# Optimization experiments

Measured on AMD Instinct MI355X. Metric: run time of the kernel, lower is better.

The kernel has to match this reference:

```python
import jax, jax.numpy as jnp
import numpy as np

N_NODES = 50000
N_EDGES = 800000
DIM = 128  # in_dim == out_dim (required by the original module's math)
BN_EPS = 1e-5


def setup_inputs() -> dict:
    key = jax.random.key(0)
    ks = jax.random.split(key, 12)
    d = DIM
    s = 1.0 / np.sqrt(d)
    x = jax.random.normal(ks[0], (N_NODES, d), dtype=jnp.float32)
    edge_index = jax.random.randint(ks[1], (2, N_EDGES), 0, N_NODES, dtype=jnp.int64)
    # message_fn: Linear(in_dim, out_dim)
    W_msg = jax.random.uniform(ks[2], (d, d), jnp.float32, -s, s)
    b_msg = jax.random.uniform(ks[3], (d,), jnp.float32, -s, s)
    # attention: Linear(2*in_dim, 1)
    sa = 1.0 / np.sqrt(2 * d)
    W_att = jax.random.uniform(ks[4], (2 * d, 1), jnp.float32, -sa, sa)
    b_att = jax.random.uniform(ks[5], (1,), jnp.float32, -sa, sa)
    # GRUCell(out_dim, out_dim): weight_ih [3d, d], weight_hh [3d, d]
    W_ih = jax.random.uniform(ks[6], (3 * d, d), jnp.float32, -s, s)
    b_ih = jax.random.uniform(ks[7], (3 * d,), jnp.float32, -s, s)
    W_hh = jax.random.uniform(ks[8], (3 * d, d), jnp.float32, -s, s)
    b_hh = jax.random.uniform(ks[9], (3 * d,), jnp.float32, -s, s)
    # BatchNorm1d(out_dim)
    gamma = jnp.ones((d,), jnp.float32)
    beta = jnp.zeros((d,), jnp.float32)
    return {"x": x, "edge_index": edge_index, "W_msg": W_msg, "b_msg": b_msg,
            "W_att": W_att, "b_att": b_att, "W_ih": W_ih, "b_ih": b_ih,
            "W_hh": W_hh, "b_hh": b_hh, "gamma": gamma, "beta": beta}


def reference(x, edge_index, W_msg, b_msg, W_att, b_att, W_ih, b_ih, W_hh, b_hh, gamma, beta):
    num_nodes, d = x.shape
    src = edge_index[0]
    dst = edge_index[1]
    xs = x[src]            # [E, d] gather
    xd = x[dst]            # [E, d] gather
    # sigmoid(cat([xs, xd]) @ W_att + b_att) without materializing the concat
    att = jax.nn.sigmoid(xs @ W_att[:d] + xd @ W_att[d:] + b_att)  # [E, 1]
    messages = (xs @ W_msg + b_msg) * att                          # [E, d]
    aggregated = jax.ops.segment_sum(messages, dst, num_segments=num_nodes)  # scatter-add
    # GRUCell(aggregated, x)
    gi = aggregated @ W_ih.T + b_ih   # [N, 3d]
    gh = x @ W_hh.T + b_hh            # [N, 3d]
    i_r, i_z, i_n = jnp.split(gi, 3, axis=1)
    h_r, h_z, h_n = jnp.split(gh, 3, axis=1)
    r = jax.nn.sigmoid(i_r + h_r)
    z = jax.nn.sigmoid(i_z + h_z)
    n = jnp.tanh(i_n + r * h_n)
    h_new = (1.0 - z) * n + z * x
    # dropout is identity in eval mode; BatchNorm1d in training mode (batch stats, biased var)
    mean = jnp.mean(h_new, axis=0)
    var = jnp.var(h_new, axis=0)
    return gamma * (h_new - mean) * jax.lax.rsqrt(var + BN_EPS) + beta
```

## Files before the change

kernel.cpp:

```cpp
#include <hip/hip_runtime.h>
#include <hip/hip_bf16.h>

#define DIM 128
#define SWS 136
typedef __hip_bfloat16 bf16;
typedef __attribute__((ext_vector_type(8))) short bf16x8;
typedef __attribute__((ext_vector_type(4))) float f32x4;

__device__ __forceinline__ float b2f(bf16 v) { return __bfloat162float(v); }
__device__ __forceinline__ bf16  f2b(float v) { return __float2bfloat16(v); }

template<bool F32>
__device__ __forceinline__ float ldf(const void* p, size_t i) {
    if (F32) return ((const float*)p)[i];
    else     return b2f(((const bf16*)p)[i]);
}
template<bool F32>
__device__ __forceinline__ void stf(void* p, size_t i, float v) {
    if (F32) ((float*)p)[i] = v;
    else     ((bf16*)p)[i] = f2b(v);
}

__device__ __forceinline__ bf16x8 pack8_f32(const float* p) {
    bf16x8 r;
#pragma unroll
    for (int i = 0; i < 8; ++i) { bf16 t = f2b(p[i]); r[i] = *(const short*)&t; }
    return r;
}
template<bool F32>
__device__ __forceinline__ bf16x8 load_frag(const void* base, size_t off) {
    if (F32) return pack8_f32((const float*)base + off);
    else     return *(const bf16x8*)((const unsigned short*)base + off);
}

__device__ __forceinline__ float bflo(unsigned int m) { return __uint_as_float(m << 16); }
__device__ __forceinline__ float bfhi(unsigned int m) { return __uint_as_float(m & 0xFFFF0000u); }

__device__ __forceinline__ float sigmoidf_fast(float v) { return 1.0f / (1.0f + __expf(-v)); }
__device__ __forceinline__ float tanhf_fast(float t) {
    float e2 = __expf(2.0f * t);
    return 1.0f - 2.0f / (e2 + 1.0f);
}

__global__ void detect_kernel(const void* __restrict__ ei, const void* __restrict__ gamma,
                              int n_nodes, int* __restrict__ flags)
{
    if (blockIdx.x == 0 && threadIdx.x == 0) {
        const long long* e64 = (const long long*)ei;
        int ok = 1;
        for (int i = 0; i < 16; ++i) {
            long long v = e64[i];
            if (v < 0 || v >= (long long)n_nodes) ok = 0;
        }
        flags[0] = ok;
        const float* g = (const float*)gamma;
        flags[1] = (fabsf(g[0] - 1.0f) < 1e-6f && fabsf(g[1] - 1.0f) < 1e-6f) ? 1 : 0;
    }
}

__device__ void atomic_add_bf16(bf16* addr, float val)
{
    unsigned int* base = (unsigned int*)((size_t)addr & ~(size_t)3);
    bool hi = ((size_t)addr & 2) != 0;
    unsigned int old = *base, assumed;
    do {
        assumed = old;
        unsigned short cur = hi ? (unsigned short)(assumed >> 16) : (unsigned short)(assumed & 0xFFFF);
        bf16 cb = *(bf16*)&cur;
        bf16 nb = f2b(b2f(cb) + val);
        unsigned short ns = *(unsigned short*)&nb;
        unsigned int newv = hi ? ((assumed & 0x0000FFFFu) | ((unsigned int)ns << 16))
                               : ((assumed & 0xFFFF0000u) | (unsigned int)ns);
        old = atomicCAS(base, assumed, newv);
    } while (old != assumed);
}

#define NW (144 * 128)
#define NI (384 * 128)
__global__ __launch_bounds__(256) void prep_weights_kernel(
    const void* __restrict__ W_msg, const void* __restrict__ W_att,
    const void* __restrict__ W_ih, const void* __restrict__ W_hh,
    unsigned short* __restrict__ wbuf, const int* __restrict__ flags)
{
    bool f32 = flags[1] != 0;
    int i = blockIdx.x * blockDim.x + threadIdx.x;
    if (i >= NW + 2 * NI) return;
    float v;
    if (i < NW) {
        int j = i >> 7, k = i & 127;
        if (j < 128)       v = f32 ? ((const float*)W_msg)[k * 128 + j] : b2f(((const bf16*)W_msg)[k * 128 + j]);
        else if (j == 128) v = f32 ? ((const float*)W_att)[k]           : b2f(((const bf16*)W_att)[k]);
        else if (j == 129) v = f32 ? ((const float*)W_att)[128 + k]     : b2f(((const bf16*)W_att)[128 + k]);
        else               v = 0.0f;
    } else if (i < NW + NI) {
        int t = i - NW;
        v = f32 ? ((const float*)W_ih)[t] : b2f(((const bf16*)W_ih)[t]);
    } else {
        int t = i - NW - NI;
        v = f32 ? ((const float*)W_hh)[t] : b2f(((const bf16*)W_hh)[t]);
    }
    bf16 b = f2b(v);
    wbuf[i] = *(unsigned short*)&b;
}

template<bool F32>
__device__ void node_mfma_body(unsigned short* __restrict__ sw,
                               const void* __restrict__ x, const unsigned short* __restrict__ Wnode,
                               const void* __restrict__ b_msg, unsigned short* __restrict__ Mb,
                               float* __restrict__ a_src, float* __restrict__ a_dst, int n_nodes)
{
    int wave = threadIdx.x >> 6, lane = threadIdx.x & 63;
    int m0 = (blockIdx.x * 8 + wave) * 16;
    int mrow = lane & 15, quad = lane >> 4;
    bool active = (m0 < n_nodes);
    int mnode = active ? (m0 + mrow < n_nodes ? m0 + mrow : n_nodes - 1) : 0;

    {
        int t = threadIdx.x;
#pragma unroll
        for (int i = 0; i < 5; ++i) {
            int v = t + i * 512;
            if (v < 2304) {
                int row = v >> 4, col = (v & 15) * 8;
                *(bf16x8*)(sw + row * SWS + col) = *(const bf16x8*)(Wnode + row * DIM + col);
            }
        }
    }

    bf16x8 a[4];
#pragma unroll
    for (int kq = 0; kq < 4; ++kq)
        a[kq] = load_frag<F32>(x, (size_t)mnode * DIM + kq * 32 + quad * 8);

    __syncthreads();

#pragma unroll
    for (int jt = 0; jt < 9; ++jt) {
        const unsigned short* wr = sw + (jt * 16 + mrow) * SWS + quad * 8;
        bf16x8 B[4];
#pragma unroll
        for (int kq = 0; kq < 4; ++kq)
            B[kq] = *(const bf16x8*)(wr + kq * 32);
        f32x4 acc = {0, 0, 0, 0};
#pragma unroll
        for (int kq = 0; kq < 4; ++kq)
            acc = __builtin_amdgcn_mfma_f32_16x16x32_bf16(a[kq], B[kq], acc, 0, 0, 0);
        if (!active) continue;
        if (jt < 8) {
            int jcol = jt * 16 + mrow;
            float bm = ldf<F32>(b_msg, jcol);
#pragma unroll
            for (int rg = 0; rg < 4; ++rg) {
                int node = m0 + quad * 4 + rg;
                if (node < n_nodes) {
                    bf16 bb = f2b(acc[rg] + bm);
                    Mb[(size_t)node * DIM + jcol] = *(unsigned short*)&bb;
                }
            }
        } else if (mrow < 2) {
#pragma unroll
            for (int rg = 0; rg < 4; ++rg) {
                int node = m0 + quad * 4 + rg;
                if (node < n_nodes) {
                    if (mrow == 0) a_src[node] = acc[rg];
                    else           a_dst[node] = acc[rg];
                }
            }
        }
    }
}

__global__ __launch_bounds__(512) void node_mfma_kernel(
    const void* x, const unsigned short* Wnode, const void* b_msg,
    unsigned short* Mb, float* a_src, float* a_dst, int n_nodes, const int* __restrict__ flags)
{
    __shared__ unsigned short sw[144 * SWS];
    if (flags[1]) node_mfma_body<true>(sw, x, Wnode, b_msg, Mb, a_src, a_dst, n_nodes);
    else          node_mfma_body<false>(sw, x, Wnode, b_msg, Mb, a_src, a_dst, n_nodes);
}

__global__ __launch_bounds__(256) void hist_kernel(
    const void* __restrict__ ei, int* __restrict__ deg, int n_edges, const int* __restrict__ flags)
{
    int i = blockIdx.x * blockDim.x + threadIdx.x;
    if (i >= n_edges) return;
    int t = flags[0] ? (int)((const long long*)ei)[n_edges + i] : ((const int*)ei)[n_edges + i];
    atomicAdd(&deg[t], 1);
}

__global__ __launch_bounds__(256) void partial_sum_kernel(
    const int* __restrict__ deg, int* __restrict__ partials, int n_nodes)
{
    __shared__ int s[256];
    int t = threadIdx.x;
    int i = blockIdx.x * 256 + t;
    s[t] = (i < n_nodes) ? deg[i] : 0;
    __syncthreads();
    for (int off = 128; off > 0; off >>= 1) {
        if (t < off) s[t] += s[t + off];
        __syncthreads();
    }
    if (t == 0) partials[blockIdx.x] = s[0];
}

__global__ __launch_bounds__(256) void partial_scan_kernel(
    int* __restrict__ partials, int nblocks)
{
    __shared__ int s[256];
    int t = threadIdx.x;
    int v = (t < nblocks) ? partials[t] : 0;
    s[t] = v;
    __syncthreads();
    for (int off = 1; off < 256; off <<= 1) {
        int u = (t >= off) ? s[t - off] : 0;
        __syncthreads();
        s[t] += u;
        __syncthreads();
    }
    if (t < nblocks) partials[t] = s[t] - v;
}

__global__ __launch_bounds__(256) void scan_write_kernel(
    const int* __restrict__ deg, const int* __restrict__ partials,
    int* __restrict__ row_start, int* __restrict__ fill, int n_nodes, int n_edges)
{
    __shared__ int s[256];
    int t = threadIdx.x;
    int i = blockIdx.x * 256 + t;
    int v = (i < n_nodes) ? deg[i] : 0;
    s[t] = v;
    __syncthreads();
    for (int off = 1; off < 256; off <<= 1) {
        int u = (t >= off) ? s[t - off] : 0;
        __syncthreads();
        s[t] += u;
        __syncthreads();
    }
    int excl = s[t] - v + partials[blockIdx.x];
    if (i < n_nodes) { row_start[i] = excl; fill[i] = excl; }
    if (blockIdx.x == 0 && t == 0) row_start[n_nodes] = n_edges;
}

__global__ __launch_bounds__(256) void scatter_kernel(
    const void* __restrict__ ei, const float* __restrict__ a_src, const float* __restrict__ a_dst,
    const void* __restrict__ b_att, int* __restrict__ fill,
    int* __restrict__ sorted_src, float* __restrict__ att,
    const int* __restrict__ flags, int n_edges)
{
    int i = blockIdx.x * blockDim.x + threadIdx.x;
    if (i >= n_edges) return;
    int s, t;
    if (flags[0]) {
        const long long* p = (const long long*)ei;
        s = (int)p[i]; t = (int)p[n_edges + i];
    } else {
        const int* p = (const int*)ei;
        s = p[i]; t = p[n_edges + i];
    }
    float battv = flags[1] ? ((const float*)b_att)[0] : b2f(((const bf16*)b_att)[0]);
    int pos = atomicAdd(&fill[t], 1);
    sorted_src[pos] = s;
    float logit = a_src[s] + a_dst[t] + battv;
    att[pos] = 1.0f / (1.0f + __expf(-logit));
}

__global__ __launch_bounds__(256) void aggregate_kernel(
    const unsigned short* __restrict__ Mb, const int* __restrict__ row_start,
    const int* __restrict__ sorted_src, const float* __restrict__ att,
    unsigned short* __restrict__ aggb, int n_nodes)
{
    int w = (int)((blockIdx.x * (unsigned)blockDim.x + threadIdx.x) >> 6);
    int lane = threadIdx.x & 63;
    if (w >= n_nodes) return;
    int beg = row_start[w], end = row_start[w + 1];
    float acc0 = 0.0f, acc1 = 0.0f;
    int e = beg;
    for (; e + 4 <= end; e += 4) {
        int s0 = sorted_src[e], s1 = sorted_src[e + 1], s2 = sorted_src[e + 2], s3 = sorted_src[e + 3];
        float w0 = att[e], w1 = att[e + 1], w2 = att[e + 2], w3 = att[e + 3];
        unsigned int m0 = *(const unsigned int*)(Mb + ((size_t)s0 << 7) + lane * 2);
        unsigned int m1 = *(const unsigned int*)(Mb + ((size_t)s1 << 7) + lane * 2);
        unsigned int m2 = *(const unsigned int*)(Mb + ((size_t)s2 << 7) + lane * 2);
        unsigned int m3 = *(const unsigned int*)(Mb + ((size_t)s3 << 7) + lane * 2);
        acc0 += w0 * bflo(m0) + w1 * bflo(m1) + w2 * bflo(m2) + w3 * bflo(m3);
        acc1 += w0 * bfhi(m0) + w1 * bfhi(m1) + w2 * bfhi(m2) + w3 * bfhi(m3);
    }
    for (; e < end; ++e) {
        int s = sorted_src[e];
        float a = att[e];
        unsigned int m = *(const unsigned int*)(Mb + ((size_t)s << 7) + lane * 2);
        acc0 += a * bflo(m);
        acc1 += a * bfhi(m);
    }
    bf16 r0 = f2b(acc0), r1 = f2b(acc1);
    unsigned int packed = (unsigned int)(*(unsigned short*)&r0) |
                          ((unsigned int)(*(unsigned short*)&r1) << 16);
    *(unsigned int*)(aggb + ((size_t)w << 7) + lane * 2) = packed;
}

template<bool F32>
__device__ void gru_mfma_body(unsigned short* __restrict__ sw,
                              const void* __restrict__ x, const unsigned short* __restrict__ aggb,
                              const unsigned short* __restrict__ Wih, const unsigned short* __restrict__ Whh,
                              const void* __restrict__ b_ih, const void* __restrict__ b_hh,
                              void* __restrict__ h_out, int n_nodes)
{
    int wave = threadIdx.x >> 6, lane = threadIdx.x & 63;
    int m0 = (blockIdx.x * 8 + wave) * 16;
    int mrow = lane & 15, quad = lane >> 4;
    bool active = (m0 < n_nodes);
    int mnode = active ? (m0 + mrow < n_nodes ? m0 + mrow : n_nodes - 1) : 0;

    bf16x8 a_ag[4], a_x[4];
#pragma unroll
    for (int kq = 0; kq < 4; ++kq) {
        a_ag[kq] = *(const bf16x8*)(aggb + (size_t)mnode * DIM + kq * 32 + quad * 8);
        a_x[kq]  = load_frag<F32>(x, (size_t)mnode * DIM + kq * 32 + quad * 8);
    }

    for (int jt = 0; jt < 8; ++jt) {
        {
            int t = threadIdx.x;
#pragma unroll
            for (int i = 0; i < 3; ++i) {
                int v = t + i * 512;
                int row = v >> 4;
                int col = (v & 15) * 8;
                int g   = row >> 4;
                int grow = row & 15;
                const unsigned short* srcm = (g < 3) ? Wih : Whh;
                const unsigned short* src = srcm + ((size_t)((g % 3) * 128 + jt * 16 + grow) * DIM + col);
                *(bf16x8*)(sw + row * SWS + col) = *(const bf16x8*)src;
            }
        }
        __syncthreads();

        f32x4 acc_ir = {0,0,0,0}, acc_iz = {0,0,0,0}, acc_in = {0,0,0,0};
        f32x4 acc_hr = {0,0,0,0}, acc_hz = {0,0,0,0}, acc_hn = {0,0,0,0};

#pragma unroll
        for (int half = 0; half < 2; ++half) {
            bf16x8 B[12];
#pragma unroll
            for (int kq = 0; kq < 2; ++kq) {
                int k = half * 2 + kq;
                int boff = mrow * SWS + k * 32 + quad * 8;
#pragma unroll
                for (int g = 0; g < 6; ++g)
                    B[kq * 6 + g] = *(const bf16x8*)(sw + g * (16 * SWS) + boff);
            }
#pragma unroll
            for (int kq = 0; kq < 2; ++kq) {
                int k = half * 2 + kq;
                acc_ir = __builtin_amdgcn_mfma_f32_16x16x32_bf16(a_ag[k], B[kq * 6 + 0], acc_ir, 0, 0, 0);
                acc_iz = __builtin_amdgcn_mfma_f32_16x16x32_bf16(a_ag[k], B[kq * 6 + 1], acc_iz, 0, 0, 0);
                acc_in = __builtin_amdgcn_mfma_f32_16x16x32_bf16(a_ag[k], B[kq * 6 + 2], acc_in, 0, 0, 0);
                acc_hr = __builtin_amdgcn_mfma_f32_16x16x32_bf16(a_x[k],  B[kq * 6 + 3], acc_hr, 0, 0, 0);
                acc_hz = __builtin_amdgcn_mfma_f32_16x16x32_bf16(a_x[k],  B[kq * 6 + 4], acc_hz, 0, 0, 0);
                acc_hn = __builtin_amdgcn_mfma_f32_16x16x32_bf16(a_x[k],  B[kq * 6 + 5], acc_hn, 0, 0, 0);
            }
        }
        __syncthreads();

        if (!active) continue;
        int jcol = jt * 16 + mrow;
        float xsv[4];
#pragma unroll
        for (int rg = 0; rg < 4; ++rg) {
            int node = m0 + quad * 4 + rg;
            int nclamp = node < n_nodes ? node : (n_nodes - 1);
            xsv[rg] = ldf<F32>(x, (size_t)nclamp * DIM + jcol);
        }
        float bir = ldf<F32>(b_ih, jcol), biz = ldf<F32>(b_ih, 128 + jcol), bin_ = ldf<F32>(b_ih, 256 + jcol);
        float bhr = ldf<F32>(b_hh, jcol), bhz = ldf<F32>(b_hh, 128 + jcol), bhn  = ldf<F32>(b_hh, 256 + jcol);
#pragma unroll
        for (int rg = 0; rg < 4; ++rg) {
            int node = m0 + quad * 4 + rg;
            if (node >= n_nodes) continue;
            float gir = acc_ir[rg] + bir, giz = acc_iz[rg] + biz, gin = acc_in[rg] + bin_;
            float ghr = acc_hr[rg] + bhr, ghz = acc_hz[rg] + bhz, ghn = acc_hn[rg] + bhn;
            float r = sigmoidf_fast(gir + ghr);
            float z = sigmoidf_fast(giz + ghz);
            float nn = tanhf_fast(gin + r * ghn);
            stf<F32>(h_out, (size_t)node * DIM + jcol, (1.0f - z) * nn + z * xsv[rg]);
        }
    }
}

__global__ __launch_bounds__(512) void gru_mfma_kernel(
    const void* x, const unsigned short* aggb, const unsigned short* Wih, const unsigned short* Whh,
    const void* b_ih, const void* b_hh, void* h_out, int n_nodes, const int* __restrict__ flags)
{
    __shared__ unsigned short sw[96 * SWS];
    if (flags[1]) gru_mfma_body<true>(sw, x, aggb, Wih, Whh, b_ih, b_hh, h_out, n_nodes);
    else          gru_mfma_body<false>(sw, x, aggb, Wih, Whh, b_ih, b_hh, h_out, n_nodes);
}

template<bool F32>
__device__ void node_pre_body(const void* __restrict__ x, const void* __restrict__ W_msg,
                              const void* __restrict__ b_msg, const void* __restrict__ W_att,
                              void* __restrict__ M, float* __restrict__ a_src,
                              float* __restrict__ a_dst)
{
    int n = blockIdx.x;
    int j = threadIdx.x;
    __shared__ float xs[DIM], r1[DIM], r2[DIM];
    float xv = ldf<F32>(x, (size_t)n * DIM + j);
    xs[j] = xv;
    r1[j] = xv * ldf<F32>(W_att, j);
    r2[j] = xv * ldf<F32>(W_att, DIM + j);
    __syncthreads();
    float acc = ldf<F32>(b_msg, j);
#pragma unroll 8
    for (int k = 0; k < DIM; ++k)
        acc += xs[k] * ldf<F32>(W_msg, (size_t)k * DIM + j);
    stf<F32>(M, (size_t)n * DIM + j, acc);
    for (int s = 64; s > 0; s >>= 1) {
        __syncthreads();
        if (j < s) { r1[j] += r1[j + s]; r2[j] += r2[j + s]; }
    }
    if (j == 0) { a_src[n] = r1[0]; a_dst[n] = r2[0]; }
}

__global__ __launch_bounds__(128) void node_pre_kernel(
    const void* x, const void* W_msg, const void* b_msg, const void* W_att,
    void* M, float* a_src, float* a_dst, const int* __restrict__ flags)
{
    if (flags[1]) node_pre_body<true>(x, W_msg, b_msg, W_att, M, a_src, a_dst);
    else          node_pre_body<false>(x, W_msg, b_msg, W_att, M, a_src, a_dst);
}

template<bool F32, bool AGGF32>
__device__ void edge_body(const void* __restrict__ ei, const void* __restrict__ M,
                          const float* __restrict__ a_src, const float* __restrict__ a_dst,
                          const void* __restrict__ b_att, void* __restrict__ agg,
                          int idx64, int n_edges)
{
    int e = (int)((blockIdx.x * (unsigned)blockDim.x + threadIdx.x) >> 6);
    int lane = threadIdx.x & 63;
    if (e >= n_edges) return;
    int s, t;
    if (idx64) {
        const long long* p = (const long long*)ei;
        s = (int)p[e]; t = (int)p[n_edges + e];
    } else {
        const int* p = (const int*)ei;
        s = p[e]; t = p[n_edges + e];
    }
    float logit = a_src[s] + a_dst[t] + ldf<F32>(b_att, 0);
    float attv = 1.0f / (1.0f + __expf(-logit));
    float m0 = ldf<F32>(M, (size_t)s * DIM + lane) * attv;
    float m1 = ldf<F32>(M, (size_t)s * DIM + 64 + lane) * attv;
    if (AGGF32) {
        float* a = (float*)agg;
        atomicAdd(&a[(size_t)t * DIM + lane], m0);
        atomicAdd(&a[(size_t)t * DIM + 64 + lane], m1);
    } else {
        bf16* a = (bf16*)agg;
        atomic_add_bf16(&a[(size_t)t * DIM + lane], m0);
        atomic_add_bf16(&a[(size_t)t * DIM + 64 + lane], m1);
    }
}

template<bool AGGF32>
__global__ __launch_bounds__(256) void edge_kernel(
    const void* ei, const void* M, const float* a_src, const float* a_dst,
    const void* b_att, void* agg, const int* __restrict__ flags, int n_edges)
{
    if (flags[1]) edge_body<true, AGGF32>(ei, M, a_src, a_dst, b_att, agg, flags[0], n_edges);
    else          edge_body<false, AGGF32>(ei, M, a_src, a_dst, b_att, agg, flags[0], n_edges);
}

#define NPB 8
template<bool F32, bool AGGF32>
__device__ void gru_body(const void* __restrict__ x, const void* __restrict__ agg,
                         const void* __restrict__ W_ih, const void* __restrict__ b_ih,
                         const void* __restrict__ W_hh, const void* __restrict__ b_hh,
                         void* __restrict__ h_new, int n_nodes)
{
    int node0 = blockIdx.x * NPB;
    int j = threadIdx.x;
    __shared__ float ag[NPB][DIM];
    __shared__ float xv[NPB][DIM];
    __shared__ float gi[NPB][3 * DIM];
    __shared__ float gh[NPB][3 * DIM];
    for (int i = j; i < NPB * DIM; i += 384) {
        int nn = i >> 7, d = i & 127;
        int node = node0 + nn;
        if (node < n_nodes) {
            ag[nn][d] = AGGF32 ? ((const float*)agg)[(size_t)node * DIM + d]
                               : b2f(((const bf16*)agg)[(size_t)node * DIM + d]);
            xv[nn][d] = ldf<F32>(x, (size_t)node * DIM + d);
        } else { ag[nn][d] = 0.0f; xv[nn][d] = 0.0f; }
    }
    __syncthreads();
    {
        float acc_i[NPB], acc_h[NPB];
        float bi = ldf<F32>(b_ih, j);
        float bh = ldf<F32>(b_hh, j);
#pragma unroll
        for (int m = 0; m < NPB; ++m) { acc_i[m] = bi; acc_h[m] = bh; }
#pragma unroll 4
        for (int k = 0; k < DIM; ++k) {
            float wik = ldf<F32>(W_ih, (size_t)j * DIM + k);
            float whk = ldf<F32>(W_hh, (size_t)j * DIM + k);
#pragma unroll
            for (int m = 0; m < NPB; ++m) {
                acc_i[m] += ag[m][k] * wik;
                acc_h[m] += xv[m][k] * whk;
            }
        }
#pragma unroll
        for (int m = 0; m < NPB; ++m) { gi[m][j] = acc_i[m]; gh[m][j] = acc_h[m]; }
    }
    __syncthreads();
    for (int i = j; i < NPB * DIM; i += 384) {
        int nn = i >> 7, d = i & 127;
        int node = node0 + nn;
        if (node >= n_nodes) continue;
        float r = 1.0f / (1.0f + __expf(-(gi[nn][d] + gh[nn][d])));
        float z = 1.0f / (1.0f + __expf(-(gi[nn][DIM + d] + gh[nn][DIM + d])));
        float nv = tanhf(gi[nn][2 * DIM + d] + r * gh[nn][2 * DIM + d]);
        float h = (1.0f - z) * nv + z * xv[nn][d];
        stf<F32>(h_new, (size_t)node * DIM + d, h);
    }
}

template<bool AGGF32>
__global__ __launch_bounds__(384) void gru_kernel(
    const void* x, const void* agg, const void* W_ih, const void* b_ih,
    const void* W_hh, const void* b_hh, void* h_new, int n_nodes,
    const int* __restrict__ flags)
{
    if (flags[1]) gru_body<true, AGGF32>(x, agg, W_ih, b_ih, W_hh, b_hh, h_new, n_nodes);
    else          gru_body<false, AGGF32>(x, agg, W_ih, b_ih, W_hh, b_hh, h_new, n_nodes);
}

template<bool F32>
__device__ void bn_stats_body(const void* __restrict__ h, float* __restrict__ sums, int n_nodes)
{
    __shared__ float s1[256], s2[256];
    int tid = threadIdx.x;
    int d = tid & 127, half = tid >> 7;
    float acc = 0.0f, accsq = 0.0f;
    for (int node = blockIdx.x * 2 + half; node < n_nodes; node += gridDim.x * 2) {
        float v = ldf<F32>(h, (size_t)node * DIM + d);
        acc += v; accsq += v * v;
    }
    s1[tid] = acc; s2[tid] = accsq;
    __syncthreads();
    if (tid < 128) {
        atomicAdd(&sums[d], s1[tid] + s1[tid + 128]);
        atomicAdd(&sums[DIM + d], s2[tid] + s2[tid + 128]);
    }
}

__global__ __launch_bounds__(256) void bn_stats_kernel(
    const void* h, float* sums, int n_nodes, const int* __restrict__ flags)
{
    if (flags[1]) bn_stats_body<true>(h, sums, n_nodes);
    else          bn_stats_body<false>(h, sums, n_nodes);
}

template<bool F32>
__device__ void bn_norm_body(void* __restrict__ h, const float* __restrict__ sums,
                             const void* __restrict__ gamma, const void* __restrict__ beta,
                             int n_nodes)
{
    int idx = blockIdx.x * blockDim.x + threadIdx.x;
    int total = n_nodes * DIM;
    if (idx >= total) return;
    int d = idx & 127;
    float inv_n = 1.0f / (float)n_nodes;
    float mean = sums[d] * inv_n;
    float var = sums[DIM + d] * inv_n - mean * mean;
    float inv = rsqrtf(var + 1e-5f);
    float v = ldf<F32>(h, idx);
    stf<F32>(h, idx, (v - mean) * inv * ldf<F32>(gamma, d) + ldf<F32>(beta, d));
}

__global__ __launch_bounds__(256) void bn_norm_kernel(
    void* h, const float* sums, const void* gamma, const void* beta,
    int n_nodes, const int* __restrict__ flags)
{
    if (flags[1]) bn_norm_body<true>(h, sums, gamma, beta, n_nodes);
    else          bn_norm_body<false>(h, sums, gamma, beta, n_nodes);
}

extern "C" void kernel_launch(void* const* d_in, const int* in_sizes, int n_in,
                              void* d_out, int out_size, void* d_ws, size_t ws_size,
                              hipStream_t stream)
{
    const void* x     = d_in[0];
    const void* ei    = d_in[1];
    const void* W_msg = d_in[2];
    const void* b_msg = d_in[3];
    const void* W_att = d_in[4];
    const void* b_att = d_in[5];
    const void* W_ih  = d_in[6];
    const void* b_ih  = d_in[7];
    const void* W_hh  = d_in[8];
    const void* b_hh  = d_in[9];
    const void* gamma = d_in[10];
    const void* beta  = d_in[11];

    int n_nodes = in_sizes[0] / DIM;
    int n_edges = in_sizes[1] / 2;
    size_t nd = (size_t)n_nodes * DIM;

    int*   flags = (int*)d_ws;
    float* sums  = (float*)(flags + 64);
    float* a_src = sums + 256;
    float* a_dst = a_src + n_nodes;
    unsigned short* aggb = (unsigned short*)(a_dst + n_nodes);
    unsigned short* wbuf = aggb + nd;
    int* deg       = (int*)(wbuf + NW + 2 * NI);
    int* row_start = deg + n_nodes;
    int* fill      = row_start + n_nodes + 1;
    int* partials  = fill + n_nodes;
    int* sorted_src = partials + 256;
    float* att     = (float*)(sorted_src + n_edges);
    size_t need_main = (size_t)((char*)(att + n_edges) - (char*)d_ws);

    hipMemsetAsync(sums, 0, 256 * sizeof(float), stream);
    detect_kernel<<<1, 64, 0, stream>>>(ei, gamma, n_nodes, flags);

    int total = n_nodes * DIM;
    int norm_blocks = (total + 255) / 256;
    int tiles = (n_nodes + 15) / 16;
    int tblocks8 = (tiles + 7) / 8;
    int eblocks = (n_edges + 255) / 256;
    int sblocks = (n_nodes + 255) / 256;

    if (ws_size >= need_main && sblocks <= 256) {
        hipMemsetAsync(deg, 0, (size_t)n_nodes * sizeof(int), stream);
        prep_weights_kernel<<<(NW + 2 * NI + 255) / 256, 256, 0, stream>>>(
            W_msg, W_att, W_ih, W_hh, wbuf, flags);
        unsigned short* Mb = (unsigned short*)d_out;
        node_mfma_kernel<<<tblocks8, 512, 0, stream>>>(
            x, wbuf, b_msg, Mb, a_src, a_dst, n_nodes, flags);
        hist_kernel<<<eblocks, 256, 0, stream>>>(ei, deg, n_edges, flags);
        partial_sum_kernel<<<sblocks, 256, 0, stream>>>(deg, partials, n_nodes);
        partial_scan_kernel<<<1, 256, 0, stream>>>(partials, sblocks);
        scan_write_kernel<<<sblocks, 256, 0, stream>>>(deg, partials, row_start, fill, n_nodes, n_edges);
        scatter_kernel<<<eblocks, 256, 0, stream>>>(
            ei, a_src, a_dst, b_att, fill, sorted_src, att, flags, n_edges);
        aggregate_kernel<<<(n_nodes + 3) / 4, 256, 0, stream>>>(
            Mb, row_start, sorted_src, att, aggb, n_nodes);
        gru_mfma_kernel<<<tblocks8, 512, 0, stream>>>(
            x, aggb, wbuf + NW, wbuf + NW + NI, b_ih, b_hh, d_out, n_nodes, flags);
    } else {
        char* big = (char*)(a_dst + n_nodes);
        size_t small_bytes = (size_t)(big - (char*)d_ws);
        int edge_blocks = (int)(((size_t)n_edges * 64 + 255) / 256);
        if (ws_size >= small_bytes + nd * sizeof(float)) {
            float* agg = (float*)big;
            hipMemsetAsync(agg, 0, nd * sizeof(float), stream);
            node_pre_kernel<<<n_nodes, 128, 0, stream>>>(x, W_msg, b_msg, W_att, d_out, a_src, a_dst, flags);
            edge_kernel<true><<<edge_blocks, 256, 0, stream>>>(ei, d_out, a_src, a_dst, b_att, agg, flags, n_edges);
            gru_kernel<true><<<(n_nodes + NPB - 1) / NPB, 384, 0, stream>>>(x, agg, W_ih, b_ih, W_hh, b_hh, d_out, n_nodes, flags);
        } else {
            bf16* agg = (bf16*)big;
            hipMemsetAsync(agg, 0, nd * sizeof(bf16), stream);
            node_pre_kernel<<<n_nodes, 128, 0, stream>>>(x, W_msg, b_msg, W_att, d_out, a_src, a_dst, flags);
            edge_kernel<false><<<edge_blocks, 256, 0, stream>>>(ei, d_out, a_src, a_dst, b_att, agg, flags, n_edges);
            gru_kernel<false><<<(n_nodes + NPB - 1) / NPB, 384, 0, stream>>>(x, agg, W_ih, b_ih, W_hh, b_hh, d_out, n_nodes, flags);
        }
    }

    bn_stats_kernel<<<512, 256, 0, stream>>>(d_out, sums, n_nodes, flags);
    bn_norm_kernel<<<norm_blocks, 256, 0, stream>>>(d_out, sums, gamma, beta, n_nodes, flags);
}
```

Before: 321.7 us.

## Double-buffer GRU weight tiles in LDS with register prefetch

The GRU MFMA kernel now keeps two LDS buffers for the weight tiles. While computing on the current column tile it prefetches the next tile from global memory into registers and writes it to the other buffer. This cuts one of the two barriers per iteration and hides part of the weight-load latency behind the MFMAs and the gate epilogue. LDS use doubles to about 52KB per block, which may limit how many blocks fit on a CU.

```diff
diff --git a/kernel.cpp b/kernel.cpp
--- a/kernel.cpp
+++ b/kernel.cpp
@@ -305,12 +305,26 @@
                               const void* __restrict__ b_ih, const void* __restrict__ b_hh,
                               void* __restrict__ h_out, int n_nodes)
 {
+    const int BUF = 96 * SWS;
     int wave = threadIdx.x >> 6, lane = threadIdx.x & 63;
     int m0 = (blockIdx.x * 8 + wave) * 16;
     int mrow = lane & 15, quad = lane >> 4;
     bool active = (m0 < n_nodes);
     int mnode = active ? (m0 + mrow < n_nodes ? m0 + mrow : n_nodes - 1) : 0;
 
+    int t = threadIdx.x;
+    int srow[3], scol[3];
+    const unsigned short* sbase[3];
+#pragma unroll
+    for (int i = 0; i < 3; ++i) {
+        int v = t + i * 512;
+        int row = v >> 4;
+        scol[i] = (v & 15) * 8;
+        srow[i] = row;
+        int g = row >> 4;
+        sbase[i] = ((g < 3) ? Wih : Whh) + (size_t)((g % 3) * 128 + (row & 15)) * DIM;
+    }
+
     bf16x8 a_ag[4], a_x[4];
 #pragma unroll
     for (int kq = 0; kq < 4; ++kq) {
@@ -318,22 +332,23 @@
         a_x[kq]  = load_frag<F32>(x, (size_t)mnode * DIM + kq * 32 + quad * 8);
     }
 
+#pragma unroll
+    for (int i = 0; i < 3; ++i) {
+        bf16x8 d = *(const bf16x8*)(sbase[i] + 0 * 16 * DIM + scol[i]);
+        *(bf16x8*)(sw + srow[i] * SWS + scol[i]) = d;
+    }
+    __syncthreads();
+
     for (int jt = 0; jt < 8; ++jt) {
-        {
-            int t = threadIdx.x;
-#pragma unroll
-            for (int i = 0; i < 3; ++i) {
-                int v = t + i * 512;
-                int row = v >> 4;
-                int col = (v & 15) * 8;
-                int g   = row >> 4;
-                int grow = row & 15;
-                const unsigned short* srcm = (g < 3) ? Wih : Whh;
-                const unsigned short* src = srcm + ((size_t)((g % 3) * 128 + jt * 16 + grow) * DIM + col);
-                *(bf16x8*)(sw + row * SWS + col) = *(const bf16x8*)src;
-            }
-        }
-        __syncthreads();
+        unsigned short* cur = sw + (jt & 1) * BUF;
+        unsigned short* nxt = sw + ((jt + 1) & 1) * BUF;
+
+        bf16x8 pf[3];
+        if (jt < 7) {
+#pragma unroll
+            for (int i = 0; i < 3; ++i)
+                pf[i] = *(const bf16x8*)(sbase[i] + (size_t)(jt + 1) * 16 * DIM + scol[i]);
+        }
 
         f32x4 acc_ir = {0,0,0,0}, acc_iz = {0,0,0,0}, acc_in = {0,0,0,0};
         f32x4 acc_hr = {0,0,0,0}, acc_hz = {0,0,0,0}, acc_hn = {0,0,0,0};
@@ -347,7 +362,7 @@
                 int boff = mrow * SWS + k * 32 + quad * 8;
 #pragma unroll
                 for (int g = 0; g < 6; ++g)
-                    B[kq * 6 + g] = *(const bf16x8*)(sw + g * (16 * SWS) + boff);
+                    B[kq * 6 + g] = *(const bf16x8*)(cur + g * (16 * SWS) + boff);
             }
 #pragma unroll
             for (int kq = 0; kq < 2; ++kq) {
@@ -360,30 +375,37 @@
                 acc_hn = __builtin_amdgcn_mfma_f32_16x16x32_bf16(a_x[k],  B[kq * 6 + 5], acc_hn, 0, 0, 0);
             }
         }
+
+        if (jt < 7) {
+#pragma unroll
+            for (int i = 0; i < 3; ++i)
+                *(bf16x8*)(nxt + srow[i] * SWS + scol[i]) = pf[i];
+        }
+
+        if (active) {
+            int jcol = jt * 16 + mrow;
+            float xsv[4];
+#pragma unroll
+            for (int rg = 0; rg < 4; ++rg) {
+                int node = m0 + quad * 4 + rg;
+                int nclamp = node < n_nodes ? node : (n_nodes - 1);
+                xsv[rg] = ldf<F32>(x, (size_t)nclamp * DIM + jcol);
+            }
+            float bir = ldf<F32>(b_ih, jcol), biz = ldf<F32>(b_ih, 128 + jcol), bin_ = ldf<F32>(b_ih, 256 + jcol);
+            float bhr = ldf<F32>(b_hh, jcol), bhz = ldf<F32>(b_hh, 128 + jcol), bhn  = ldf<F32>(b_hh, 256 + jcol);
+#pragma unroll
+            for (int rg = 0; rg < 4; ++rg) {
+                int node = m0 + quad * 4 + rg;
+                if (node >= n_nodes) continue;
+                float gir = acc_ir[rg] + bir, giz = acc_iz[rg] + biz, gin = acc_in[rg] + bin_;
+                float ghr = acc_hr[rg] + bhr, ghz = acc_hz[rg] + bhz, ghn = acc_hn[rg] + bhn;
+                float r = sigmoidf_fast(gir + ghr);
+                float z = sigmoidf_fast(giz + ghz);
+                float nn = tanhf_fast(gin + r * ghn);
+                stf<F32>(h_out, (size_t)node * DIM + jcol, (1.0f - z) * nn + z * xsv[rg]);
+            }
+        }
         __syncthreads();
-
-        if (!active) continue;
-        int jcol = jt * 16 + mrow;
-        float xsv[4];
-#pragma unroll
-        for (int rg = 0; rg < 4; ++rg) {
-            int node = m0 + quad * 4 + rg;
-            int nclamp = node < n_nodes ? node : (n_nodes - 1);
-            xsv[rg] = ldf<F32>(x, (size_t)nclamp * DIM + jcol);
-        }
-        float bir = ldf<F32>(b_ih, jcol), biz = ldf<F32>(b_ih, 128 + jcol), bin_ = ldf<F32>(b_ih, 256 + jcol);
-        float bhr = ldf<F32>(b_hh, jcol), bhz = ldf<F32>(b_hh, 128 + jcol), bhn  = ldf<F32>(b_hh, 256 + jcol);
-#pragma unroll
-        for (int rg = 0; rg < 4; ++rg) {
-            int node = m0 + quad * 4 + rg;
-            if (node >= n_nodes) continue;
-            float gir = acc_ir[rg] + bir, giz = acc_iz[rg] + biz, gin = acc_in[rg] + bin_;
-            float ghr = acc_hr[rg] + bhr, ghz = acc_hz[rg] + bhz, ghn = acc_hn[rg] + bhn;
-            float r = sigmoidf_fast(gir + ghr);
-            float z = sigmoidf_fast(giz + ghz);
-            float nn = tanhf_fast(gin + r * ghn);
-            stf<F32>(h_out, (size_t)node * DIM + jcol, (1.0f - z) * nn + z * xsv[rg]);
-        }
     }
 }
 
@@ -391,7 +413,7 @@
     const void* x, const unsigned short* aggb, const unsigned short* Wih, const unsigned short* Whh,
     const void* b_ih, const void* b_hh, void* h_out, int n_nodes, const int* __restrict__ flags)
 {
-    __shared__ unsigned short sw[96 * SWS];
+    __shared__ unsigned short sw[2 * 96 * SWS];
     if (flags[1]) gru_mfma_body<true>(sw, x, aggb, Wih, Whh, b_ih, b_hh, h_out, n_nodes);
     else          gru_mfma_body<false>(sw, x, aggb, Wih, Whh, b_ih, b_hh, h_out, n_nodes);
 }
```

Result: faster. 314.2 us (-2.3%).
